# Kernel tuning notes

Measured on AMD Instinct MI355X. Metric: run time of the kernel, lower is better.

The kernel has to match this reference:

```python
import jax, jax.numpy as jnp
import numpy as np

B, S, D, H, A = 4, 2048, 512, 8, 64


def setup_inputs() -> dict:
    key = jax.random.key(0)
    ks = jax.random.split(key, 12)
    inv_d = 1.0 / np.sqrt(D)
    inv_ha = 1.0 / np.sqrt(H * A)
    return {
        "query": jax.random.normal(ks[0], (B, S, D), jnp.float32),
        "key": jax.random.normal(ks[1], (B, S, D), jnp.float32),
        "value": jax.random.normal(ks[2], (B, S, D), jnp.float32),
        # stacked per-head projection weights, layout [H, in, out] so y = x @ W + b
        "Wq": jax.random.uniform(ks[3], (H, D, A), jnp.float32, -inv_d, inv_d),
        "bq": jax.random.uniform(ks[4], (H, A), jnp.float32, -inv_d, inv_d),
        "Wk": jax.random.uniform(ks[5], (H, D, A), jnp.float32, -inv_d, inv_d),
        "bk": jax.random.uniform(ks[6], (H, A), jnp.float32, -inv_d, inv_d),
        "Wv": jax.random.uniform(ks[7], (H, D, A), jnp.float32, -inv_d, inv_d),
        "bv": jax.random.uniform(ks[8], (H, A), jnp.float32, -inv_d, inv_d),
        "Wo": jax.random.uniform(ks[9], (H * A, D), jnp.float32, -inv_ha, inv_ha),
        "bo": jax.random.uniform(ks[10], (D,), jnp.float32, -inv_ha, inv_ha),
    }


def reference(query, key, value, Wq, bq, Wk, bk, Wv, bv, Wo, bo):
    b, s, _ = query.shape
    h, _, a = Wq.shape
    # per-head projections, batched across heads: [B,H,S,A]
    q = jnp.einsum("bsd,hda->bhsa", query, Wq) + bq[None, :, None, :]
    k = jnp.einsum("bsd,hda->bhsa", key, Wk) + bk[None, :, None, :]
    v = jnp.einsum("bsd,hda->bhsa", value, Wv) + bv[None, :, None, :]
    scale = a ** 0.5
    scores = jnp.einsum("bhqa,bhka->bhqk", q, k) / scale  # [B,H,S,S]
    # Faithful to original: subsequent_mask has 0.0 on lower tri, -inf above;
    # masked_fill(mask == 0, -1e9) therefore masks the LOWER triangle (incl diag).
    tril = jnp.tril(jnp.ones((s, s), dtype=bool))
    scores = jnp.where(tril, jnp.float32(-1e9), scores)
    attn = jax.nn.softmax(scores, axis=-1)
    out = jnp.einsum("bhqk,bhka->bhqa", attn, v)  # [B,H,S,A]
    # concat heads in order (head-major in feature dim, matching torch.cat dim=-1)
    out = out.transpose(0, 2, 1, 3).reshape(b, s, h * a)
    return out @ Wo + bo
```

## Files before the change

kernel.cpp:

```cpp
#include <hip/hip_runtime.h>
#include <hip/hip_bf16.h>

#define B_ 4
#define S_ 2048
#define D_ 512
#define H_ 8
#define A_ 64

typedef __attribute__((ext_vector_type(8))) __bf16 bf16x8;
typedef __attribute__((ext_vector_type(4))) __bf16 bf16x4;
typedef __attribute__((ext_vector_type(4))) float f32x4;

static __device__ __forceinline__ f32x4 mfma16(bf16x8 a, bf16x8 b, f32x4 c) {
  return __builtin_amdgcn_mfma_f32_16x16x32_bf16(a, b, c, 0, 0, 0);
}

static __device__ __forceinline__ f32x4 zero4() {
  f32x4 z = {0.f, 0.f, 0.f, 0.f};
  return z;
}

#define QSCALE 0.18033688011f

#if __has_builtin(__builtin_amdgcn_exp2f)
#define EXP2(x) __builtin_amdgcn_exp2f(x)
#else
#define EXP2(x) exp2f(x)
#endif

#define GLDS(g, l)                                                      \
  __builtin_amdgcn_global_load_lds(                                     \
      (const __attribute__((address_space(1))) void*)(g),               \
      (__attribute__((address_space(3))) void*)(l), 16, 0, 0)

__global__ void prep_all_kernel(const float* __restrict__ q, const float* __restrict__ k,
                                const float* __restrict__ v,
                                const float* __restrict__ Wq, const float* __restrict__ Wk,
                                const float* __restrict__ Wv, const float* __restrict__ Wo,
                                __bf16* __restrict__ xq, __bf16* __restrict__ xk,
                                __bf16* __restrict__ xv,
                                __bf16* __restrict__ tq, __bf16* __restrict__ tk,
                                __bf16* __restrict__ tv, __bf16* __restrict__ to_) {
  __shared__ float tile[64][65];
  if (blockIdx.x < 12288) {
    int idx = blockIdx.x * 256 + threadIdx.x;
    int which = idx >> 20;
    int i = idx & ((1 << 20) - 1);
    const float4* s = (const float4*)(which == 0 ? q : (which == 1 ? k : v));
    __bf16* d = (which == 0) ? xq : (which == 1 ? xk : xv);
    float4 f = s[i];
    bf16x4 o;
    o.x = (__bf16)f.x; o.y = (__bf16)f.y; o.z = (__bf16)f.z; o.w = (__bf16)f.w;
    *(bf16x4*)(d + 4 * i) = o;
  } else {
    int t = blockIdx.x - 12288;
    if (t < 192) {
      int mat = t >> 6;
      int h = (t >> 3) & 7;
      int d0 = (t & 7) * 64;
      const float* W = (mat == 0) ? Wq : (mat == 1 ? Wk : Wv);
      __bf16* dst = (mat == 0) ? tq : (mat == 1 ? tk : tv);
      float sc = (mat == 0) ? QSCALE : 1.0f;
      int a = threadIdx.x & 63, r0 = threadIdx.x >> 6;
#pragma unroll
      for (int i = 0; i < 16; i++) {
        int dd = r0 * 16 + i;
        tile[dd][a] = W[(h * D_ + d0 + dd) * A_ + a] * sc;
      }
      __syncthreads();
      int dd = threadIdx.x & 63, a0 = threadIdx.x >> 6;
#pragma unroll
      for (int i = 0; i < 16; i++) {
        int a2 = a0 * 16 + i;
        dst[(h * 64 + a2) * D_ + d0 + dd] = (__bf16)tile[dd][a2];
      }
    } else {
      int t2 = t - 192;
      int f0 = (t2 >> 3) * 64, d0 = (t2 & 7) * 64;
      int d = threadIdx.x & 63, r0 = threadIdx.x >> 6;
#pragma unroll
      for (int i = 0; i < 16; i++) {
        int ff = r0 * 16 + i;
        tile[ff][d] = Wo[(f0 + ff) * D_ + d0 + d];
      }
      __syncthreads();
      int f = threadIdx.x & 63, a0 = threadIdx.x >> 6;
#pragma unroll
      for (int i = 0; i < 16; i++) {
        int dd = a0 * 16 + i;
        to_[(d0 + dd) * D_ + f0 + f] = (__bf16)tile[f][dd];
      }
    }
  }
}

__global__ __launch_bounds__(256) void proj_gemm_kernel(
    const __bf16* __restrict__ Xq, const __bf16* __restrict__ Xk, const __bf16* __restrict__ Xv,
    const __bf16* __restrict__ Wtq, const __bf16* __restrict__ Wtk, const __bf16* __restrict__ Wtv,
    const float* __restrict__ bq, const float* __restrict__ bk, const float* __restrict__ bv,
    __bf16* __restrict__ Qb, __bf16* __restrict__ Kb, __bf16* __restrict__ Vtb) {
  int z = blockIdx.z;
  const __bf16* X  = (z == 0) ? Xq  : (z == 1 ? Xk  : Xv);
  const __bf16* Wt = (z == 0) ? Wtq : (z == 1 ? Wtk : Wtv);
  const float* bias = (z == 0) ? bq : (z == 1 ? bk : bv);
  float bscale = (z == 0) ? QSCALE : 1.0f;

  int lane = threadIdx.x & 63, wv = threadIdx.x >> 6;
  int wr = wv >> 1, wc = wv & 1;
  int quad = lane >> 4, lc = lane & 15;
  int M0 = blockIdx.x * 128, N0 = blockIdx.y * 128;
  int m0 = M0 + wr * 64, n0 = N0 + wc * 64;

  __shared__ __align__(16) __bf16 smem[2 * 2 * 128 * 64];
#define AB(buf) (smem + (buf) * 16384)
#define BB(buf) (smem + (buf) * 16384 + 8192)

  int srow = lane >> 3;
  int sg = ((lane & 7) ^ srow) * 8;

#pragma unroll
  for (int i = 0; i < 4; ++i) {
    int r0 = wv * 32 + i * 8;
    GLDS(X  + (M0 + r0 + srow) * D_ + sg, AB(0) + r0 * 64);
    GLDS(Wt + (N0 + r0 + srow) * D_ + sg, BB(0) + r0 * 64);
  }

  f32x4 acc[4][4];
#pragma unroll
  for (int mt = 0; mt < 4; mt++)
#pragma unroll
    for (int nt = 0; nt < 4; nt++) acc[mt][nt] = zero4();

  __syncthreads();

  for (int j = 0; j < 8; ++j) {
    int cb = j & 1;
    if (j < 7) {
      int k0 = (j + 1) * 64;
#pragma unroll
      for (int i = 0; i < 4; ++i) {
        int r0 = wv * 32 + i * 8;
        GLDS(X  + (M0 + r0 + srow) * D_ + k0 + sg, AB(cb ^ 1) + r0 * 64);
        GLDS(Wt + (N0 + r0 + srow) * D_ + k0 + sg, BB(cb ^ 1) + r0 * 64);
      }
    }
    const __bf16* Al = AB(cb);
    const __bf16* Bl = BB(cb);
#pragma unroll
    for (int kk = 0; kk < 2; ++kk) {
      int gp = ((kk * 4 + quad) ^ (lc & 7)) * 8;
      bf16x8 a[4], bb[4];
#pragma unroll
      for (int mt = 0; mt < 4; mt++)
        a[mt] = *(const bf16x8*)(Al + (wr * 64 + mt * 16 + lc) * 64 + gp);
#pragma unroll
      for (int nt = 0; nt < 4; nt++)
        bb[nt] = *(const bf16x8*)(Bl + (wc * 64 + nt * 16 + lc) * 64 + gp);
#pragma unroll
      for (int mt = 0; mt < 4; mt++)
#pragma unroll
        for (int nt = 0; nt < 4; nt++)
          acc[mt][nt] = mfma16(a[mt], bb[nt], acc[mt][nt]);
    }
    __syncthreads();
  }

  __bf16* vlds = smem + wv * (64 * 72);

  int h = n0 >> 6;
  int b = m0 >> 11, s0 = m0 & (S_ - 1);
  if (z < 2) {
#pragma unroll
    for (int nt = 0; nt < 4; nt++) {
      int col = n0 + nt * 16 + lc;
      float bval = bias[col] * bscale;
#pragma unroll
      for (int mt = 0; mt < 4; mt++)
#pragma unroll
        for (int r = 0; r < 4; r++)
          vlds[(mt * 16 + quad * 4 + r) * 72 + nt * 16 + lc] = (__bf16)(acc[mt][nt][r] + bval);
    }
    __asm__ volatile("s_waitcnt lgkmcnt(0)" ::: "memory");
    __bf16* dst = (z == 0) ? Qb : Kb;
#pragma unroll
    for (int it = 0; it < 8; it++) {
      int row = it * 8 + (lane >> 3);
      int c8 = (lane & 7) * 8;
      bf16x8 vv = *(const bf16x8*)(vlds + row * 72 + c8);
      *(bf16x8*)(dst + ((b * H_ + h) * S_ + s0 + row) * A_ + c8) = vv;
    }
  } else {
#pragma unroll
    for (int nt = 0; nt < 4; nt++) {
      int col = n0 + nt * 16 + lc;
      float bval = bias[col];
#pragma unroll
      for (int mt = 0; mt < 4; mt++) {
        bf16x4 pk;
#pragma unroll
        for (int r = 0; r < 4; r++) pk[r] = (__bf16)(acc[mt][nt][r] + bval);
        *(bf16x4*)(vlds + (nt * 16 + lc) * 72 + mt * 16 + quad * 4) = pk;
      }
    }
    __asm__ volatile("s_waitcnt lgkmcnt(0)" ::: "memory");
#pragma unroll
    for (int it = 0; it < 8; it++) {
      int a_l = it * 8 + (lane >> 3);
      int s_l = (lane & 7) * 8;
      bf16x8 vvv = *(const bf16x8*)(vlds + a_l * 72 + s_l);
      *(bf16x8*)(Vtb + ((b * H_ + h) * A_ + a_l) * S_ + s0 + s_l) = vvv;
    }
  }
}

__global__ __launch_bounds__(256, 4) void flash_kernel(const __bf16* __restrict__ Q,
                                                       const __bf16* __restrict__ K,
                                                       const __bf16* __restrict__ Vt,
                                                       __bf16* __restrict__ O) {
  int id = blockIdx.x;
  int xcd = id & 7, slot = id >> 3;
  int pair = slot & 31, half = slot >> 5;
  int pr = pair >> 1;
  int beta = half ? (15 - pr) : pr;
  int bh = xcd * 4 + (pair & 1) + 2 * half;
  int lane = threadIdx.x & 63, wv = threadIdx.x >> 6;
  int quad = lane >> 4, lc = lane & 15;
  int R0 = beta * 128 + wv * 32;
  int ntile = 32 - 2 * beta;
  int t0 = 2 * beta;

  const __bf16* Qp = Q + bh * S_ * A_;
  const __bf16* Kp = K + bh * S_ * A_;
  const __bf16* Vp = Vt + bh * A_ * S_;

  __shared__ __align__(16) __bf16 kvbuf[2][2][64][64];
  __shared__ __align__(16) __bf16 plds_all[4][32][72];
  __bf16* plds = &plds_all[wv][0][0];

  int srow = lane >> 3;
  int sg = ((lane & 7) ^ srow) * 8;

  {
    int kt = t0 << 6;
#pragma unroll
    for (int i = 0; i < 2; ++i) {
      int r0 = wv * 16 + i * 8;
      GLDS(Kp + (kt + r0 + srow) * A_ + sg, &kvbuf[0][0][r0][0]);
      GLDS(Vp + (r0 + srow) * S_ + kt + sg, &kvbuf[0][1][r0][0]);
    }
  }

  bf16x8 qf[2][2];
#pragma unroll
  for (int qt = 0; qt < 2; qt++) {
    qf[qt][0] = *(const bf16x8*)(Qp + (R0 + qt * 16 + lc) * A_ + quad * 8);
    qf[qt][1] = *(const bf16x8*)(Qp + (R0 + qt * 16 + lc) * A_ + 32 + quad * 8);
  }

  f32x4 o[2][4];
  float lsum[2][4];
#pragma unroll
  for (int qt = 0; qt < 2; qt++)
#pragma unroll
    for (int t = 0; t < 4; t++) { o[qt][t] = zero4(); lsum[qt][t] = 0.f; }

  int g0 = (quad ^ (lc & 7)) * 8;
  int g1 = ((quad + 4) ^ (lc & 7)) * 8;

  __syncthreads();

  for (int j = 0; j < ntile; ++j) {
    int t = t0 + j;
    int cb = j & 1;
    if (j + 1 < ntile) {
      int ktn = (t + 1) << 6;
#pragma unroll
      for (int i = 0; i < 2; ++i) {
        int r0 = wv * 16 + i * 8;
        GLDS(Kp + (ktn + r0 + srow) * A_ + sg, &kvbuf[cb ^ 1][0][r0][0]);
        GLDS(Vp + (r0 + srow) * S_ + ktn + sg, &kvbuf[cb ^ 1][1][r0][0]);
      }
    }
    bool skip = (t * 64 + 63 <= R0);
    if (!skip) {
      const __bf16* Kl = &kvbuf[cb][0][0][0];
      const __bf16* Vl = &kvbuf[cb][1][0][0];
      f32x4 sc[2][4];
#pragma unroll
      for (int nt = 0; nt < 4; nt++) {
        int rr = nt * 16 + lc;
        bf16x8 kf0 = *(const bf16x8*)(Kl + rr * 64 + g0);
        bf16x8 kf1 = *(const bf16x8*)(Kl + rr * 64 + g1);
#pragma unroll
        for (int qt = 0; qt < 2; qt++) {
          f32x4 ss = zero4();
          ss = mfma16(qf[qt][0], kf0, ss);
          ss = mfma16(qf[qt][1], kf1, ss);
          sc[qt][nt] = ss;
        }
      }
      if (t * 64 < R0 + 32) {
#pragma unroll
        for (int qt = 0; qt < 2; qt++)
#pragma unroll
          for (int nt = 0; nt < 4; nt++) {
            int col = t * 64 + nt * 16 + lc;
#pragma unroll
            for (int r = 0; r < 4; r++) {
              int row = R0 + qt * 16 + quad * 4 + r;
              float pv = (col <= row) ? 0.0f : EXP2(sc[qt][nt][r]);
              lsum[qt][r] += pv;
              plds[(qt * 16 + quad * 4 + r) * 72 + nt * 16 + lc] = (__bf16)pv;
            }
          }
      } else {
#pragma unroll
        for (int qt = 0; qt < 2; qt++)
#pragma unroll
          for (int nt = 0; nt < 4; nt++)
#pragma unroll
            for (int r = 0; r < 4; r++) {
              float pv = EXP2(sc[qt][nt][r]);
              lsum[qt][r] += pv;
              plds[(qt * 16 + quad * 4 + r) * 72 + nt * 16 + lc] = (__bf16)pv;
            }
      }
      __asm__ volatile("s_waitcnt lgkmcnt(0)" ::: "memory");
      bf16x8 pf[2][2];
#pragma unroll
      for (int qt = 0; qt < 2; qt++) {
        pf[qt][0] = *(const bf16x8*)(plds + (qt * 16 + lc) * 72 + quad * 8);
        pf[qt][1] = *(const bf16x8*)(plds + (qt * 16 + lc) * 72 + 32 + quad * 8);
      }
      __builtin_amdgcn_s_setprio(1);
#pragma unroll
      for (int ot = 0; ot < 4; ot++) {
        int rr = ot * 16 + lc;
        bf16x8 vf0 = *(const bf16x8*)(Vl + rr * 64 + g0);
        bf16x8 vf1 = *(const bf16x8*)(Vl + rr * 64 + g1);
#pragma unroll
        for (int qt = 0; qt < 2; qt++) {
          o[qt][ot] = mfma16(pf[qt][0], vf0, o[qt][ot]);
          o[qt][ot] = mfma16(pf[qt][1], vf1, o[qt][ot]);
        }
      }
      __builtin_amdgcn_s_setprio(0);
    }
    __syncthreads();
  }

#pragma unroll
  for (int qt = 0; qt < 2; qt++)
#pragma unroll
    for (int r = 0; r < 4; r++) {
      float l = lsum[qt][r];
#pragma unroll
      for (int off = 1; off < 16; off <<= 1) l += __shfl_xor(l, off, 64);
      lsum[qt][r] = l;
    }

#pragma unroll
  for (int qt = 0; qt < 2; qt++)
#pragma unroll
    for (int r = 0; r < 4; r++) {
      float rl = 1.0f / lsum[qt][r];
#pragma unroll
      for (int ot = 0; ot < 4; ot++)
        plds[(qt * 16 + quad * 4 + r) * 72 + ot * 16 + lc] = (__bf16)(o[qt][ot][r] * rl);
    }
  __asm__ volatile("s_waitcnt lgkmcnt(0)" ::: "memory");
  int b = bh >> 3, h = bh & 7;
#pragma unroll
  for (int it = 0; it < 4; it++) {
    int row = it * 8 + (lane >> 3);
    int c8 = (lane & 7) * 8;
    int grow = R0 + row;
    if (grow != S_ - 1)
      *(bf16x8*)(O + (b * S_ + grow) * (H_ * A_) + h * 64 + c8) =
          *(const bf16x8*)(plds + row * 72 + c8);
  }

  if (beta == 15) {
    int a = threadIdx.x >> 2;
    int li = threadIdx.x & 3;
    const __bf16* src = Vp + a * S_;
    float ssum = 0.f;
#pragma unroll 8
    for (int j2 = 0; j2 < 64; j2++) {
      bf16x8 vv = *(const bf16x8*)(src + (j2 * 4 + li) * 8);
#pragma unroll
      for (int e = 0; e < 8; e++) ssum += (float)vv[e];
    }
    ssum += __shfl_xor(ssum, 1, 64);
    ssum += __shfl_xor(ssum, 2, 64);
    if (li == 0)
      O[(b * S_ + (S_ - 1)) * (H_ * A_) + h * 64 + a] = (__bf16)(ssum * (1.0f / 2048.0f));
  }
}

__global__ __launch_bounds__(256) void out_gemm_kernel(const __bf16* __restrict__ Ob,
                                                       const __bf16* __restrict__ Wot,
                                                       const float* __restrict__ bo,
                                                       float* __restrict__ out) {
  int lane = threadIdx.x & 63, wv = threadIdx.x >> 6;
  int wr = wv >> 1, wc = wv & 1;
  int quad = lane >> 4, lc = lane & 15;
  int M0 = blockIdx.x * 128, N0 = blockIdx.y * 128;
  int m0 = M0 + wr * 64, n0 = N0 + wc * 64;

  __shared__ __align__(16) __bf16 smem[2 * 2 * 128 * 64];

  int srow = lane >> 3;
  int sg = ((lane & 7) ^ srow) * 8;

#pragma unroll
  for (int i = 0; i < 4; ++i) {
    int r0 = wv * 32 + i * 8;
    GLDS(Ob  + (M0 + r0 + srow) * D_ + sg, AB(0) + r0 * 64);
    GLDS(Wot + (N0 + r0 + srow) * D_ + sg, BB(0) + r0 * 64);
  }

  f32x4 acc[4][4];
#pragma unroll
  for (int mt = 0; mt < 4; mt++)
#pragma unroll
    for (int nt = 0; nt < 4; nt++) acc[mt][nt] = zero4();

  __syncthreads();

  for (int j = 0; j < 8; ++j) {
    int cb = j & 1;
    if (j < 7) {
      int k0 = (j + 1) * 64;
#pragma unroll
      for (int i = 0; i < 4; ++i) {
        int r0 = wv * 32 + i * 8;
        GLDS(Ob  + (M0 + r0 + srow) * D_ + k0 + sg, AB(cb ^ 1) + r0 * 64);
        GLDS(Wot + (N0 + r0 + srow) * D_ + k0 + sg, BB(cb ^ 1) + r0 * 64);
      }
    }
    const __bf16* Al = AB(cb);
    const __bf16* Bl = BB(cb);
#pragma unroll
    for (int kk = 0; kk < 2; ++kk) {
      int gp = ((kk * 4 + quad) ^ (lc & 7)) * 8;
      bf16x8 a[4], bb[4];
#pragma unroll
      for (int mt = 0; mt < 4; mt++)
        a[mt] = *(const bf16x8*)(Al + (wr * 64 + mt * 16 + lc) * 64 + gp);
#pragma unroll
      for (int nt = 0; nt < 4; nt++)
        bb[nt] = *(const bf16x8*)(Bl + (wc * 64 + nt * 16 + lc) * 64 + gp);
#pragma unroll
      for (int mt = 0; mt < 4; mt++)
#pragma unroll
        for (int nt = 0; nt < 4; nt++)
          acc[mt][nt] = mfma16(a[mt], bb[nt], acc[mt][nt]);
    }
    __syncthreads();
  }

#pragma unroll
  for (int nt = 0; nt < 4; nt++) {
    int col = n0 + nt * 16 + lc;
    float bval = bo[col];
#pragma unroll
    for (int mt = 0; mt < 4; mt++)
#pragma unroll
      for (int r = 0; r < 4; r++) {
        int row = m0 + mt * 16 + quad * 4 + r;
        out[row * D_ + col] = acc[mt][nt][r] + bval;
      }
  }
}

extern "C" void kernel_launch(void* const* d_in, const int* in_sizes, int n_in,
                              void* d_out, int out_size, void* d_ws, size_t ws_size,
                              hipStream_t stream) {
  const float* q  = (const float*)d_in[0];
  const float* k  = (const float*)d_in[1];
  const float* v  = (const float*)d_in[2];
  const float* Wq = (const float*)d_in[3];
  const float* bq = (const float*)d_in[4];
  const float* Wk = (const float*)d_in[5];
  const float* bk = (const float*)d_in[6];
  const float* Wv = (const float*)d_in[7];
  const float* bv = (const float*)d_in[8];
  const float* Wo = (const float*)d_in[9];
  const float* bo = (const float*)d_in[10];

  char* ws = (char*)d_ws;
  __bf16* Xq  = (__bf16*)(ws + 0);
  __bf16* Xk  = (__bf16*)(ws + 8388608);
  __bf16* Xv  = (__bf16*)(ws + 16777216);
  __bf16* Wtq = (__bf16*)(ws + 25165824);
  __bf16* Wtk = (__bf16*)(ws + 25690112);
  __bf16* Wtv = (__bf16*)(ws + 26214400);
  __bf16* Wot = (__bf16*)(ws + 26738688);
  __bf16* Qb  = (__bf16*)(ws + 27262976);
  __bf16* Kb  = (__bf16*)(ws + 35651584);
  __bf16* Vtb = (__bf16*)(ws + 44040192);
  __bf16* Ob  = (__bf16*)(ws + 52428800);

  prep_all_kernel<<<12544, 256, 0, stream>>>(q, k, v, Wq, Wk, Wv, Wo,
                                             Xq, Xk, Xv, Wtq, Wtk, Wtv, Wot);
  proj_gemm_kernel<<<dim3(64, 4, 3), 256, 0, stream>>>(Xq, Xk, Xv, Wtq, Wtk, Wtv,
                                                       bq, bk, bv, Qb, Kb, Vtb);
  flash_kernel<<<dim3(512), 256, 0, stream>>>(Qb, Kb, Vtb, Ob);
  out_gemm_kernel<<<dim3(64, 4), 256, 0, stream>>>(Ob, Wot, bo, (float*)d_out);
}
```

Baseline: 182.9 us.

## Pair complementary query blocks per workgroup to balance causal flash attention work

```diff
diff --git a/kernel.cpp b/kernel.cpp
--- a/kernel.cpp
+++ b/kernel.cpp
@@ -213,56 +213,48 @@
   }
 }
 
-__global__ __launch_bounds__(256, 4) void flash_kernel(const __bf16* __restrict__ Q,
-                                                       const __bf16* __restrict__ K,
-                                                       const __bf16* __restrict__ Vt,
-                                                       __bf16* __restrict__ O) {
+__global__ __launch_bounds__(512) void flash_kernel(const __bf16* __restrict__ Q,
+                                                    const __bf16* __restrict__ K,
+                                                    const __bf16* __restrict__ Vt,
+                                                    __bf16* __restrict__ O) {
   int id = blockIdx.x;
   int xcd = id & 7, slot = id >> 3;
-  int pair = slot & 31, half = slot >> 5;
-  int pr = pair >> 1;
-  int beta = half ? (15 - pr) : pr;
-  int bh = xcd * 4 + (pair & 1) + 2 * half;
+  int p = slot >> 2;
+  int bh = xcd * 4 + (slot & 3);
   int lane = threadIdx.x & 63, wv = threadIdx.x >> 6;
   int quad = lane >> 4, lc = lane & 15;
-  int R0 = beta * 128 + wv * 32;
-  int ntile = 32 - 2 * beta;
-  int t0 = 2 * beta;
+  int R1 = p * 128 + wv * 16;
+  int R2 = (15 - p) * 128 + wv * 16;
+  int t0 = 2 * p, ntile = 32 - 2 * p;
 
   const __bf16* Qp = Q + bh * S_ * A_;
   const __bf16* Kp = K + bh * S_ * A_;
   const __bf16* Vp = Vt + bh * A_ * S_;
 
   __shared__ __align__(16) __bf16 kvbuf[2][2][64][64];
-  __shared__ __align__(16) __bf16 plds_all[4][32][72];
+  __shared__ __align__(16) __bf16 plds_all[8][16][72];
   __bf16* plds = &plds_all[wv][0][0];
 
   int srow = lane >> 3;
   int sg = ((lane & 7) ^ srow) * 8;
+  int wr8 = wv * 8;
 
   {
     int kt = t0 << 6;
-#pragma unroll
-    for (int i = 0; i < 2; ++i) {
-      int r0 = wv * 16 + i * 8;
-      GLDS(Kp + (kt + r0 + srow) * A_ + sg, &kvbuf[0][0][r0][0]);
-      GLDS(Vp + (r0 + srow) * S_ + kt + sg, &kvbuf[0][1][r0][0]);
-    }
-  }
-
-  bf16x8 qf[2][2];
-#pragma unroll
-  for (int qt = 0; qt < 2; qt++) {
-    qf[qt][0] = *(const bf16x8*)(Qp + (R0 + qt * 16 + lc) * A_ + quad * 8);
-    qf[qt][1] = *(const bf16x8*)(Qp + (R0 + qt * 16 + lc) * A_ + 32 + quad * 8);
-  }
-
-  f32x4 o[2][4];
-  float lsum[2][4];
-#pragma unroll
-  for (int qt = 0; qt < 2; qt++)
-#pragma unroll
-    for (int t = 0; t < 4; t++) { o[qt][t] = zero4(); lsum[qt][t] = 0.f; }
+    GLDS(Kp + (kt + wr8 + srow) * A_ + sg, &kvbuf[0][0][wr8][0]);
+    GLDS(Vp + (wr8 + srow) * S_ + kt + sg, &kvbuf[0][1][wr8][0]);
+  }
+
+  bf16x8 qf1[2], qf2[2];
+  qf1[0] = *(const bf16x8*)(Qp + (R1 + lc) * A_ + quad * 8);
+  qf1[1] = *(const bf16x8*)(Qp + (R1 + lc) * A_ + 32 + quad * 8);
+  qf2[0] = *(const bf16x8*)(Qp + (R2 + lc) * A_ + quad * 8);
+  qf2[1] = *(const bf16x8*)(Qp + (R2 + lc) * A_ + 32 + quad * 8);
+
+  f32x4 o1[4], o2[4];
+  float ls1[4], ls2[4];
+#pragma unroll
+  for (int t = 0; t < 4; t++) { o1[t] = zero4(); o2[t] = zero4(); ls1[t] = 0.f; ls2[t] = 0.f; }
 
   int g0 = (quad ^ (lc & 7)) * 8;
   int g1 = ((quad + 4) ^ (lc & 7)) * 8;
@@ -274,75 +266,106 @@
     int cb = j & 1;
     if (j + 1 < ntile) {
       int ktn = (t + 1) << 6;
-#pragma unroll
-      for (int i = 0; i < 2; ++i) {
-        int r0 = wv * 16 + i * 8;
-        GLDS(Kp + (ktn + r0 + srow) * A_ + sg, &kvbuf[cb ^ 1][0][r0][0]);
-        GLDS(Vp + (r0 + srow) * S_ + ktn + sg, &kvbuf[cb ^ 1][1][r0][0]);
-      }
-    }
-    bool skip = (t * 64 + 63 <= R0);
-    if (!skip) {
-      const __bf16* Kl = &kvbuf[cb][0][0][0];
-      const __bf16* Vl = &kvbuf[cb][1][0][0];
-      f32x4 sc[2][4];
+      GLDS(Kp + (ktn + wr8 + srow) * A_ + sg, &kvbuf[cb ^ 1][0][wr8][0]);
+      GLDS(Vp + (wr8 + srow) * S_ + ktn + sg, &kvbuf[cb ^ 1][1][wr8][0]);
+    }
+    const __bf16* Kl = &kvbuf[cb][0][0][0];
+    const __bf16* Vl = &kvbuf[cb][1][0][0];
+
+    {
+      f32x4 sc[4];
 #pragma unroll
       for (int nt = 0; nt < 4; nt++) {
         int rr = nt * 16 + lc;
         bf16x8 kf0 = *(const bf16x8*)(Kl + rr * 64 + g0);
         bf16x8 kf1 = *(const bf16x8*)(Kl + rr * 64 + g1);
-#pragma unroll
-        for (int qt = 0; qt < 2; qt++) {
-          f32x4 ss = zero4();
-          ss = mfma16(qf[qt][0], kf0, ss);
-          ss = mfma16(qf[qt][1], kf1, ss);
-          sc[qt][nt] = ss;
+        f32x4 ss = zero4();
+        ss = mfma16(qf1[0], kf0, ss);
+        ss = mfma16(qf1[1], kf1, ss);
+        sc[nt] = ss;
+      }
+      if (t * 64 <= R1 + 15) {
+#pragma unroll
+        for (int nt = 0; nt < 4; nt++) {
+          int col = t * 64 + nt * 16 + lc;
+#pragma unroll
+          for (int r = 0; r < 4; r++) {
+            int row = R1 + quad * 4 + r;
+            float pv = (col <= row) ? 0.0f : EXP2(sc[nt][r]);
+            ls1[r] += pv;
+            plds[(quad * 4 + r) * 72 + nt * 16 + lc] = (__bf16)pv;
+          }
         }
-      }
-      if (t * 64 < R0 + 32) {
-#pragma unroll
-        for (int qt = 0; qt < 2; qt++)
-#pragma unroll
-          for (int nt = 0; nt < 4; nt++) {
-            int col = t * 64 + nt * 16 + lc;
-#pragma unroll
-            for (int r = 0; r < 4; r++) {
-              int row = R0 + qt * 16 + quad * 4 + r;
-              float pv = (col <= row) ? 0.0f : EXP2(sc[qt][nt][r]);
-              lsum[qt][r] += pv;
-              plds[(qt * 16 + quad * 4 + r) * 72 + nt * 16 + lc] = (__bf16)pv;
-            }
+      } else {
+#pragma unroll
+        for (int nt = 0; nt < 4; nt++)
+#pragma unroll
+          for (int r = 0; r < 4; r++) {
+            float pv = EXP2(sc[nt][r]);
+            ls1[r] += pv;
+            plds[(quad * 4 + r) * 72 + nt * 16 + lc] = (__bf16)pv;
           }
-      } else {
-#pragma unroll
-        for (int qt = 0; qt < 2; qt++)
-#pragma unroll
-          for (int nt = 0; nt < 4; nt++)
-#pragma unroll
-            for (int r = 0; r < 4; r++) {
-              float pv = EXP2(sc[qt][nt][r]);
-              lsum[qt][r] += pv;
-              plds[(qt * 16 + quad * 4 + r) * 72 + nt * 16 + lc] = (__bf16)pv;
-            }
       }
       __asm__ volatile("s_waitcnt lgkmcnt(0)" ::: "memory");
-      bf16x8 pf[2][2];
-#pragma unroll
-      for (int qt = 0; qt < 2; qt++) {
-        pf[qt][0] = *(const bf16x8*)(plds + (qt * 16 + lc) * 72 + quad * 8);
-        pf[qt][1] = *(const bf16x8*)(plds + (qt * 16 + lc) * 72 + 32 + quad * 8);
-      }
+      bf16x8 pf0 = *(const bf16x8*)(plds + lc * 72 + quad * 8);
+      bf16x8 pf1 = *(const bf16x8*)(plds + lc * 72 + 32 + quad * 8);
       __builtin_amdgcn_s_setprio(1);
 #pragma unroll
       for (int ot = 0; ot < 4; ot++) {
         int rr = ot * 16 + lc;
         bf16x8 vf0 = *(const bf16x8*)(Vl + rr * 64 + g0);
         bf16x8 vf1 = *(const bf16x8*)(Vl + rr * 64 + g1);
-#pragma unroll
-        for (int qt = 0; qt < 2; qt++) {
-          o[qt][ot] = mfma16(pf[qt][0], vf0, o[qt][ot]);
-          o[qt][ot] = mfma16(pf[qt][1], vf1, o[qt][ot]);
+        o1[ot] = mfma16(pf0, vf0, o1[ot]);
+        o1[ot] = mfma16(pf1, vf1, o1[ot]);
+      }
+      __builtin_amdgcn_s_setprio(0);
+    }
+
+    if (t * 64 + 63 > R2) {
+      f32x4 sc[4];
+#pragma unroll
+      for (int nt = 0; nt < 4; nt++) {
+        int rr = nt * 16 + lc;
+        bf16x8 kf0 = *(const bf16x8*)(Kl + rr * 64 + g0);
+        bf16x8 kf1 = *(const bf16x8*)(Kl + rr * 64 + g1);
+        f32x4 ss = zero4();
+        ss = mfma16(qf2[0], kf0, ss);
+        ss = mfma16(qf2[1], kf1, ss);
+        sc[nt] = ss;
+      }
+      if (t * 64 <= R2 + 15) {
+#pragma unroll
+        for (int nt = 0; nt < 4; nt++) {
+          int col = t * 64 + nt * 16 + lc;
+#pragma unroll
+          for (int r = 0; r < 4; r++) {
+            int row = R2 + quad * 4 + r;
+            float pv = (col <= row) ? 0.0f : EXP2(sc[nt][r]);
+            ls2[r] += pv;
+            plds[(quad * 4 + r) * 72 + nt * 16 + lc] = (__bf16)pv;
+          }
         }
+      } else {
+#pragma unroll
+        for (int nt = 0; nt < 4; nt++)
+#pragma unroll
+          for (int r = 0; r < 4; r++) {
+            float pv = EXP2(sc[nt][r]);
+            ls2[r] += pv;
+            plds[(quad * 4 + r) * 72 + nt * 16 + lc] = (__bf16)pv;
+          }
+      }
+      __asm__ volatile("s_waitcnt lgkmcnt(0)" ::: "memory");
+      bf16x8 pf0 = *(const bf16x8*)(plds + lc * 72 + quad * 8);
+      bf16x8 pf1 = *(const bf16x8*)(plds + lc * 72 + 32 + quad * 8);
+      __builtin_amdgcn_s_setprio(1);
+#pragma unroll
+      for (int ot = 0; ot < 4; ot++) {
+        int rr = ot * 16 + lc;
+        bf16x8 vf0 = *(const bf16x8*)(Vl + rr * 64 + g0);
+        bf16x8 vf1 = *(const bf16x8*)(Vl + rr * 64 + g1);
+        o2[ot] = mfma16(pf0, vf0, o2[ot]);
+        o2[ot] = mfma16(pf1, vf1, o2[ot]);
       }
       __builtin_amdgcn_s_setprio(0);
     }
@@ -350,49 +373,63 @@
   }
 
 #pragma unroll
-  for (int qt = 0; qt < 2; qt++)
-#pragma unroll
-    for (int r = 0; r < 4; r++) {
-      float l = lsum[qt][r];
-#pragma unroll
-      for (int off = 1; off < 16; off <<= 1) l += __shfl_xor(l, off, 64);
-      lsum[qt][r] = l;
-    }
-
-#pragma unroll
-  for (int qt = 0; qt < 2; qt++)
-#pragma unroll
-    for (int r = 0; r < 4; r++) {
-      float rl = 1.0f / lsum[qt][r];
-#pragma unroll
-      for (int ot = 0; ot < 4; ot++)
-        plds[(qt * 16 + quad * 4 + r) * 72 + ot * 16 + lc] = (__bf16)(o[qt][ot][r] * rl);
-    }
+  for (int r = 0; r < 4; r++) {
+    float l1 = ls1[r], l2 = ls2[r];
+#pragma unroll
+    for (int off = 1; off < 16; off <<= 1) { l1 += __shfl_xor(l1, off, 64); l2 += __shfl_xor(l2, off, 64); }
+    ls1[r] = l1; ls2[r] = l2;
+  }
+
+  int b = bh >> 3, h = bh & 7;
+
+#pragma unroll
+  for (int r = 0; r < 4; r++) {
+    float rl = 1.0f / ls1[r];
+#pragma unroll
+    for (int ot = 0; ot < 4; ot++)
+      plds[(quad * 4 + r) * 72 + ot * 16 + lc] = (__bf16)(o1[ot][r] * rl);
+  }
   __asm__ volatile("s_waitcnt lgkmcnt(0)" ::: "memory");
-  int b = bh >> 3, h = bh & 7;
-#pragma unroll
-  for (int it = 0; it < 4; it++) {
+#pragma unroll
+  for (int it = 0; it < 2; it++) {
     int row = it * 8 + (lane >> 3);
     int c8 = (lane & 7) * 8;
-    int grow = R0 + row;
+    *(bf16x8*)(O + (b * S_ + R1 - wv * 16 + wv * 16 + row) * (H_ * A_) + h * 64 + c8) =
+        *(const bf16x8*)(plds + row * 72 + c8);
+  }
+
+#pragma unroll
+  for (int r = 0; r < 4; r++) {
+    float rl = 1.0f / ls2[r];
+#pragma unroll
+    for (int ot = 0; ot < 4; ot++)
+      plds[(quad * 4 + r) * 72 + ot * 16 + lc] = (__bf16)(o2[ot][r] * rl);
+  }
+  __asm__ volatile("s_waitcnt lgkmcnt(0)" ::: "memory");
+#pragma unroll
+  for (int it = 0; it < 2; it++) {
+    int row = it * 8 + (lane >> 3);
+    int c8 = (lane & 7) * 8;
+    int grow = R2 + row;
     if (grow != S_ - 1)
       *(bf16x8*)(O + (b * S_ + grow) * (H_ * A_) + h * 64 + c8) =
           *(const bf16x8*)(plds + row * 72 + c8);
   }
 
-  if (beta == 15) {
-    int a = threadIdx.x >> 2;
-    int li = threadIdx.x & 3;
+  if (p == 7) {
+    int a = threadIdx.x >> 3;
+    int li = threadIdx.x & 7;
     const __bf16* src = Vp + a * S_;
     float ssum = 0.f;
 #pragma unroll 8
-    for (int j2 = 0; j2 < 64; j2++) {
-      bf16x8 vv = *(const bf16x8*)(src + (j2 * 4 + li) * 8);
+    for (int j2 = 0; j2 < 32; j2++) {
+      bf16x8 vv = *(const bf16x8*)(src + (j2 * 8 + li) * 8);
 #pragma unroll
       for (int e = 0; e < 8; e++) ssum += (float)vv[e];
     }
     ssum += __shfl_xor(ssum, 1, 64);
     ssum += __shfl_xor(ssum, 2, 64);
+    ssum += __shfl_xor(ssum, 4, 64);
     if (li == 0)
       O[(b * S_ + (S_ - 1)) * (H_ * A_) + h * 64 + a] = (__bf16)(ssum * (1.0f / 2048.0f));
   }
@@ -506,6 +543,6 @@
                                              Xq, Xk, Xv, Wtq, Wtk, Wtv, Wot);
   proj_gemm_kernel<<<dim3(64, 4, 3), 256, 0, stream>>>(Xq, Xk, Xv, Wtq, Wtk, Wtv,
                                                        bq, bk, bv, Qb, Kb, Vtb);
-  flash_kernel<<<dim3(512), 256, 0, stream>>>(Qb, Kb, Vtb, Ob);
+  flash_kernel<<<dim3(256), 512, 0, stream>>>(Qb, Kb, Vtb, Ob);
   out_gemm_kernel<<<dim3(64, 4), 256, 0, stream>>>(Ob, Wot, bo, (float*)d_out);
 }
```

New measurement: 179.5 us. About the same (-1.9%).
